# Performance work log

Measured on AMD Instinct MI355X. Metric: run time of the kernel, lower is better.

The kernel has to match this reference:

```python
import jax, jax.numpy as jnp
import numpy as np

N_NODES = 100000


def spmm(edge_src, edge_dst, edge_val, x):
    """z[dst] += val * x[src] over all edges (COO sparse-dense matmul)."""
    gathered = edge_val[:, None] * x[edge_src]  # [E, d]
    return jax.ops.segment_sum(gathered, edge_dst, num_segments=N_NODES)


def setup_inputs() -> dict:
    key = jax.random.key(0)
    k1, k2, k3, k4, k5, k6 = jax.random.split(key, 6)
    N, E, IN, H, C = N_NODES, 1600000, 256, 128, 40
    features = jax.random.normal(k1, (N, IN), dtype=jnp.float32)
    # xavier_uniform-like init
    b1 = float(np.sqrt(6.0 / (IN + H)))
    b2 = float(np.sqrt(6.0 / (H + C)))
    W1 = jax.random.uniform(k2, (IN, H), dtype=jnp.float32, minval=-b1, maxval=b1)
    W2 = jax.random.uniform(k3, (H, C), dtype=jnp.float32, minval=-b2, maxval=b2)
    edge_src = jax.random.randint(k4, (E,), 0, N, dtype=jnp.int32)
    edge_dst = jnp.sort(jax.random.randint(k5, (E,), 0, N, dtype=jnp.int32))
    # normalized-adjacency-like positive edge weights
    edge_val = jax.random.uniform(k6, (E,), dtype=jnp.float32)
    return {"features": features, "W1": W1, "W2": W2,
            "edge_src": edge_src, "edge_dst": edge_dst, "edge_val": edge_val}


def reference(features, W1, W2, edge_src, edge_dst, edge_val):
    # Decoupled GCN: all dense NN layers first (relu between, none after last) ...
    h = jax.nn.relu(features @ W1)
    h = h @ W2  # [N, num_classes]
    # ... then nlayers (=2) rounds of graph propagation (spmm aggregation)
    h = spmm(edge_src, edge_dst, edge_val, h)
    h = spmm(edge_src, edge_dst, edge_val, h)
    return h
```

## Files before the change

### kernel.cpp

```cpp
#include <hip/hip_runtime.h>
#include <cstddef>
#include <cstdint>

#define IN_DIM 256
#define H_DIM  128
#define C_DIM  40
#define BM     128
#define LDA    264
#define LDH    136
#define PAD_C  40
#define STEP   512

typedef short bf16x8 __attribute__((ext_vector_type(8)));
typedef float f32x16 __attribute__((ext_vector_type(16)));
typedef uint  u32x4  __attribute__((ext_vector_type(4)));

__device__ __forceinline__ ushort f2bf(float f) {
  uint u = __builtin_bit_cast(uint, f);
  u += 0x7fffu + ((u >> 16) & 1u);
  return (ushort)(u >> 16);
}
__device__ __forceinline__ float bf2f(uint s) {
  uint u = s << 16;
  return __builtin_bit_cast(float, u);
}
__device__ __forceinline__ uint pack2bf(float a, float b) {
#if __has_builtin(__builtin_amdgcn_cvt_pk_bf16_f32)
  typedef __bf16 bf16v2 __attribute__((ext_vector_type(2)));
  bf16v2 r = __builtin_amdgcn_cvt_pk_bf16_f32(a, b);
  return __builtin_bit_cast(uint, r);
#else
  return (uint)f2bf(a) | ((uint)f2bf(b) << 16);
#endif
}

__global__ void setup_kernel(const int* __restrict__ dst, int E,
                             int* __restrict__ row_ptr, int N,
                             const float* __restrict__ W1,
                             const float* __restrict__ W2,
                             ushort* __restrict__ b_frag,
                             ushort* __restrict__ w2f) {
  int tid = blockIdx.x * blockDim.x + threadIdx.x;
  if (tid < E) {
    int d1 = dst[tid];
    int d0 = (tid == 0) ? -1 : dst[tid - 1];
    for (int v = d0 + 1; v <= d1; ++v) row_ptr[v] = tid;
    if (tid == E - 1)
      for (int v = d1 + 1; v <= N; ++v) row_ptr[v] = E;
    return;
  }
  int u = tid - E;
  if (u < 4096) {
    int l = u & 63, ks = (u >> 6) & 15, tn = u >> 10;
    int n  = 32 * tn + (l & 31);
    int k0 = ks * 16 + ((l >> 5) << 3);
    ushort r[8];
#pragma unroll
    for (int j = 0; j < 8; ++j) r[j] = f2bf(W1[(k0 + j) * H_DIM + n]);
    *(uint4*)(b_frag + u * 8) = *(uint4*)r;
    return;
  }
  u -= 4096;
  if (u < 1024) {
    int l = u & 63, kt = u >> 6;
    int tn = kt & 1, kb = kt >> 1;
    int n  = 32 * tn + (l & 31);
    int k0 = kb * 16 + ((l >> 5) << 3);
    ushort r[8];
#pragma unroll
    for (int j = 0; j < 8; ++j)
      r[j] = (n < C_DIM) ? f2bf(W2[(k0 + j) * C_DIM + n]) : (ushort)0;
    *(uint4*)(w2f + u * 8) = *(uint4*)r;
  }
}

__global__ __launch_bounds__(256, 2) void fused_dense_kernel(
    const float* __restrict__ feat, const ushort* __restrict__ b_frag,
    const ushort* __restrict__ w2f, ushort* __restrict__ z0, int N) {
  __shared__ __align__(16) ushort smem[128 * LDA];

  const int t = threadIdx.x;
  const int w = t >> 6, l = t & 63;
  const int nb = blockIdx.x * BM;
  ushort* slab = smem + w * (32 * LDA);

  f32x16 acc[4];
#pragma unroll
  for (int tn = 0; tn < 4; ++tn)
#pragma unroll
    for (int r = 0; r < 16; ++r) acc[tn][r] = 0.f;

  const ushort* bp = b_frag + l * 8;
  bf16x8 Bx[2][4];
#pragma unroll
  for (int tn = 0; tn < 4; ++tn)
    Bx[0][tn] = *(const bf16x8*)(bp + tn * (16 * STEP));

#pragma unroll
  for (int c = 0; c < 32; ++c) {
    int grow = nb + 32 * w + c; if (grow >= N) grow = N - 1;
    float4 v = *(const float4*)(feat + (size_t)grow * IN_DIM + l * 4);
    uint2 pk;
    pk.x = pack2bf(v.x, v.y);
    pk.y = pack2bf(v.z, v.w);
    *(uint2*)(slab + c * LDA + l * 4) = pk;
  }

  const ushort* Abase = slab + (l & 31) * LDA + ((l >> 5) << 3);
#pragma unroll
  for (int ks = 0; ks < 16; ++ks) {
    const int c = ks & 1;
    if (ks < 15) {
#pragma unroll
      for (int tn = 0; tn < 4; ++tn)
        Bx[c ^ 1][tn] = *(const bf16x8*)(bp + tn * (16 * STEP) + (ks + 1) * STEP);
    }
    bf16x8 af = *(const bf16x8*)(Abase + ks * 16);
#pragma unroll
    for (int tn = 0; tn < 4; ++tn)
      acc[tn] = __builtin_amdgcn_mfma_f32_32x32x16_bf16(af, Bx[c][tn], acc[tn], 0, 0, 0);
  }

#pragma unroll
  for (int tn = 0; tn < 4; ++tn) {
    int col = tn * 32 + (l & 31);
#pragma unroll
    for (int r = 0; r < 16; ++r) {
      int nl = (r & 3) + 8 * (r >> 2) + 4 * (l >> 5);
      float v = acc[tn][r];
      slab[nl * LDH + col] = f2bf(v > 0.f ? v : 0.f);
    }
  }

  f32x16 acc2[2];
#pragma unroll
  for (int tn = 0; tn < 2; ++tn)
#pragma unroll
    for (int r = 0; r < 16; ++r) acc2[tn][r] = 0.f;

  const ushort* Hbase = slab + (l & 31) * LDH + ((l >> 5) << 3);
  const ushort* wp = w2f + l * 8;
#pragma unroll
  for (int kb = 0; kb < 8; ++kb) {
    bf16x8 af = *(const bf16x8*)(Hbase + kb * 16);
#pragma unroll
    for (int tn = 0; tn < 2; ++tn) {
      bf16x8 bfr = *(const bf16x8*)(wp + (kb * 2 + tn) * STEP);
      acc2[tn] = __builtin_amdgcn_mfma_f32_32x32x16_bf16(af, bfr, acc2[tn], 0, 0, 0);
    }
  }

#pragma unroll
  for (int tn = 0; tn < 2; ++tn) {
    int col = tn * 32 + (l & 31);
    if (col < C_DIM) {
#pragma unroll
      for (int r = 0; r < 16; ++r) {
        int node = nb + 32 * w + (r & 3) + 8 * (r >> 2) + 4 * (l >> 5);
        if (node < N) z0[(size_t)node * PAD_C + col] = f2bf(acc2[tn][r]);
      }
    }
  }
}

__global__ __launch_bounds__(256) void spmm_kernel(
    const int* __restrict__ row_ptr, const int* __restrict__ esrc,
    const float* __restrict__ eval, const ushort* __restrict__ x,
    ushort* __restrict__ zb, float* __restrict__ zf, int N, int out_f32) {
  int node = (blockIdx.x << 2) + (threadIdx.x >> 6);
  if (node >= N) return;
  const int lane = threadIdx.x & 63;
  const int h = lane >> 3;
  const int j = lane & 7;
  const bool act = (j < 5);

  int e   = row_ptr[node];
  int end = row_ptr[node + 1];

  float acc[8];
#pragma unroll
  for (int c = 0; c < 8; ++c) acc[c] = 0.f;

  for (; e + 16 <= end; e += 16) {
    int   s0 = esrc[e + h];
    int   s1 = esrc[e + 8 + h];
    float v0 = eval[e + h];
    float v1 = eval[e + 8 + h];
    if (act) {
      u32x4 a = *(const u32x4*)(x + (size_t)s0 * PAD_C + j * 8);
      u32x4 b = *(const u32x4*)(x + (size_t)s1 * PAD_C + j * 8);
      acc[0] = fmaf(v0, bf2f(a.x & 0xffffu), acc[0]);
      acc[1] = fmaf(v0, bf2f(a.x >> 16),     acc[1]);
      acc[2] = fmaf(v0, bf2f(a.y & 0xffffu), acc[2]);
      acc[3] = fmaf(v0, bf2f(a.y >> 16),     acc[3]);
      acc[4] = fmaf(v0, bf2f(a.z & 0xffffu), acc[4]);
      acc[5] = fmaf(v0, bf2f(a.z >> 16),     acc[5]);
      acc[6] = fmaf(v0, bf2f(a.w & 0xffffu), acc[6]);
      acc[7] = fmaf(v0, bf2f(a.w >> 16),     acc[7]);
      acc[0] = fmaf(v1, bf2f(b.x & 0xffffu), acc[0]);
      acc[1] = fmaf(v1, bf2f(b.x >> 16),     acc[1]);
      acc[2] = fmaf(v1, bf2f(b.y & 0xffffu), acc[2]);
      acc[3] = fmaf(v1, bf2f(b.y >> 16),     acc[3]);
      acc[4] = fmaf(v1, bf2f(b.z & 0xffffu), acc[4]);
      acc[5] = fmaf(v1, bf2f(b.z >> 16),     acc[5]);
      acc[6] = fmaf(v1, bf2f(b.w & 0xffffu), acc[6]);
      acc[7] = fmaf(v1, bf2f(b.w >> 16),     acc[7]);
    }
  }
  for (; e + 8 <= end; e += 8) {
    int   s = esrc[e + h];
    float v = eval[e + h];
    if (act) {
      u32x4 u = *(const u32x4*)(x + (size_t)s * PAD_C + j * 8);
      acc[0] = fmaf(v, bf2f(u.x & 0xffffu), acc[0]);
      acc[1] = fmaf(v, bf2f(u.x >> 16),     acc[1]);
      acc[2] = fmaf(v, bf2f(u.y & 0xffffu), acc[2]);
      acc[3] = fmaf(v, bf2f(u.y >> 16),     acc[3]);
      acc[4] = fmaf(v, bf2f(u.z & 0xffffu), acc[4]);
      acc[5] = fmaf(v, bf2f(u.z >> 16),     acc[5]);
      acc[6] = fmaf(v, bf2f(u.w & 0xffffu), acc[6]);
      acc[7] = fmaf(v, bf2f(u.w >> 16),     acc[7]);
    }
  }
  if (e < end) {
    int ei = e + h;
    int ec = ei < end ? ei : end - 1;
    int   s  = esrc[ec];
    float v0 = eval[ec];
    float v  = ei < end ? v0 : 0.f;
    if (act) {
      u32x4 u = *(const u32x4*)(x + (size_t)s * PAD_C + j * 8);
      acc[0] = fmaf(v, bf2f(u.x & 0xffffu), acc[0]);
      acc[1] = fmaf(v, bf2f(u.x >> 16),     acc[1]);
      acc[2] = fmaf(v, bf2f(u.y & 0xffffu), acc[2]);
      acc[3] = fmaf(v, bf2f(u.y >> 16),     acc[3]);
      acc[4] = fmaf(v, bf2f(u.z & 0xffffu), acc[4]);
      acc[5] = fmaf(v, bf2f(u.z >> 16),     acc[5]);
      acc[6] = fmaf(v, bf2f(u.w & 0xffffu), acc[6]);
      acc[7] = fmaf(v, bf2f(u.w >> 16),     acc[7]);
    }
  }

#pragma unroll
  for (int c = 0; c < 8; ++c) acc[c] += __shfl_xor(acc[c], 8);
#pragma unroll
  for (int c = 0; c < 8; ++c) acc[c] += __shfl_xor(acc[c], 16);
#pragma unroll
  for (int c = 0; c < 8; ++c) acc[c] += __shfl_xor(acc[c], 32);

  if (out_f32) {
    if (lane < 5) {
      float4 o0 = {acc[0], acc[1], acc[2], acc[3]};
      float4 o1 = {acc[4], acc[5], acc[6], acc[7]};
      float* p = zf + (size_t)node * C_DIM + j * 8;
      *(float4*)(p + 0) = o0;
      *(float4*)(p + 4) = o1;
    }
  } else {
    if (lane < 5) {
      uint4 p;
      p.x = (uint)f2bf(acc[0]) | ((uint)f2bf(acc[1]) << 16);
      p.y = (uint)f2bf(acc[2]) | ((uint)f2bf(acc[3]) << 16);
      p.z = (uint)f2bf(acc[4]) | ((uint)f2bf(acc[5]) << 16);
      p.w = (uint)f2bf(acc[6]) | ((uint)f2bf(acc[7]) << 16);
      *(uint4*)(zb + (size_t)node * PAD_C + j * 8) = p;
    }
  }
}

extern "C" void kernel_launch(void* const* d_in, const int* in_sizes, int n_in,
                              void* d_out, int out_size, void* d_ws, size_t ws_size,
                              hipStream_t stream) {
  const float* feat  = (const float*)d_in[0];
  const float* W1    = (const float*)d_in[1];
  const float* W2    = (const float*)d_in[2];
  const int*   esrc  = (const int*)d_in[3];
  const int*   edst  = (const int*)d_in[4];
  const float* evalp = (const float*)d_in[5];
  float* out = (float*)d_out;

  const int N = in_sizes[0] / IN_DIM;
  const int E = in_sizes[3];

  const int nblk = (N + BM - 1) / BM;

  char* ws = (char*)d_ws;
  ushort* z0     = (ushort*)ws;
  ushort* z1     = (ushort*)(ws + (size_t)N * PAD_C * 2);
  ushort* b_frag = (ushort*)(ws + (size_t)N * PAD_C * 4);
  ushort* w2f    = b_frag + 4 * 16 * STEP;
  int* row_ptr   = (int*)(w2f + 16 * STEP);

  const int setup_items = E + 4096 + 1024;
  setup_kernel<<<(setup_items + 255) / 256, 256, 0, stream>>>(
      edst, E, row_ptr, N, W1, W2, b_frag, w2f);
  fused_dense_kernel<<<nblk, 256, 0, stream>>>(feat, b_frag, w2f, z0, N);
  spmm_kernel<<<(N + 3) / 4, 256, 0, stream>>>(row_ptr, esrc, evalp, z0, z1, nullptr, N, 0);
  spmm_kernel<<<(N + 3) / 4, 256, 0, stream>>>(row_ptr, esrc, evalp, z1, nullptr, out, N, 1);
}
```

Baseline: 273.7 us.

## Split intermediate features into 64B-aligned and tail arrays; halve dense LDS footprint

The 40-column bf16 intermediate is stored as two arrays, a 32-column part (64-byte rows) and an 8-column part (16-byte rows), so each gathered row in the spmm kernels touches aligned cache-line segments instead of straddling 80-byte rows. The dense kernel now stages the feature tile in two K-halves with a smaller LDS slab, reusing it for the hidden activations, and raises the occupancy hint to 4 blocks per CU. Costs are a branch per gather lane and a second memory stream for the tail columns, plus more register pressure from the tighter launch bound.

```diff
diff --git a/kernel.cpp b/kernel.cpp
--- a/kernel.cpp
+++ b/kernel.cpp
@@ -6,9 +6,9 @@
 #define H_DIM  128
 #define C_DIM  40
 #define BM     128
-#define LDA    264
-#define LDH    136
-#define PAD_C  40
+#define LDAH   132
+#define XA_C   32
+#define XB_C   8
 #define STEP   512
 
 typedef short bf16x8 __attribute__((ext_vector_type(8)));
@@ -74,15 +74,16 @@
   }
 }
 
-__global__ __launch_bounds__(256, 2) void fused_dense_kernel(
+__global__ __launch_bounds__(256, 4) void fused_dense_kernel(
     const float* __restrict__ feat, const ushort* __restrict__ b_frag,
-    const ushort* __restrict__ w2f, ushort* __restrict__ z0, int N) {
-  __shared__ __align__(16) ushort smem[128 * LDA];
+    const ushort* __restrict__ w2f, ushort* __restrict__ z0a,
+    ushort* __restrict__ z0b, int N) {
+  __shared__ __align__(16) ushort smem[4 * 32 * LDAH];
 
   const int t = threadIdx.x;
   const int w = t >> 6, l = t & 63;
   const int nb = blockIdx.x * BM;
-  ushort* slab = smem + w * (32 * LDA);
+  ushort* slab = smem + w * (32 * LDAH);
 
   f32x16 acc[4];
 #pragma unroll
@@ -96,29 +97,34 @@
   for (int tn = 0; tn < 4; ++tn)
     Bx[0][tn] = *(const bf16x8*)(bp + tn * (16 * STEP));
 
-#pragma unroll
-  for (int c = 0; c < 32; ++c) {
-    int grow = nb + 32 * w + c; if (grow >= N) grow = N - 1;
-    float4 v = *(const float4*)(feat + (size_t)grow * IN_DIM + l * 4);
-    uint2 pk;
-    pk.x = pack2bf(v.x, v.y);
-    pk.y = pack2bf(v.z, v.w);
-    *(uint2*)(slab + c * LDA + l * 4) = pk;
-  }
-
-  const ushort* Abase = slab + (l & 31) * LDA + ((l >> 5) << 3);
-#pragma unroll
-  for (int ks = 0; ks < 16; ++ks) {
-    const int c = ks & 1;
-    if (ks < 15) {
+  const ushort* Abase = slab + (l & 31) * LDAH + ((l >> 5) << 3);
+
+#pragma unroll
+  for (int h = 0; h < 2; ++h) {
+#pragma unroll
+    for (int c = 0; c < 16; ++c) {
+      int r2 = 2 * c + (l >> 5);
+      int grow = nb + 32 * w + r2; if (grow >= N) grow = N - 1;
+      float4 v = *(const float4*)(feat + (size_t)grow * IN_DIM + h * 128 + (l & 31) * 4);
+      uint2 pk;
+      pk.x = pack2bf(v.x, v.y);
+      pk.y = pack2bf(v.z, v.w);
+      *(uint2*)(slab + r2 * LDAH + (l & 31) * 4) = pk;
+    }
+#pragma unroll
+    for (int kk = 0; kk < 8; ++kk) {
+      const int ks = h * 8 + kk;
+      const int c = ks & 1;
+      if (ks < 15) {
+#pragma unroll
+        for (int tn = 0; tn < 4; ++tn)
+          Bx[c ^ 1][tn] = *(const bf16x8*)(bp + tn * (16 * STEP) + (ks + 1) * STEP);
+      }
+      bf16x8 af = *(const bf16x8*)(Abase + kk * 16);
 #pragma unroll
       for (int tn = 0; tn < 4; ++tn)
-        Bx[c ^ 1][tn] = *(const bf16x8*)(bp + tn * (16 * STEP) + (ks + 1) * STEP);
-    }
-    bf16x8 af = *(const bf16x8*)(Abase + ks * 16);
-#pragma unroll
-    for (int tn = 0; tn < 4; ++tn)
-      acc[tn] = __builtin_amdgcn_mfma_f32_32x32x16_bf16(af, Bx[c][tn], acc[tn], 0, 0, 0);
+        acc[tn] = __builtin_amdgcn_mfma_f32_32x32x16_bf16(af, Bx[c][tn], acc[tn], 0, 0, 0);
+    }
   }
 
 #pragma unroll
@@ -128,7 +134,7 @@
     for (int r = 0; r < 16; ++r) {
       int nl = (r & 3) + 8 * (r >> 2) + 4 * (l >> 5);
       float v = acc[tn][r];
-      slab[nl * LDH + col] = f2bf(v > 0.f ? v : 0.f);
+      slab[nl * LDAH + col] = f2bf(v > 0.f ? v : 0.f);
     }
   }
 
@@ -138,7 +144,7 @@
 #pragma unroll
     for (int r = 0; r < 16; ++r) acc2[tn][r] = 0.f;
 
-  const ushort* Hbase = slab + (l & 31) * LDH + ((l >> 5) << 3);
+  const ushort* Hbase = slab + (l & 31) * LDAH + ((l >> 5) << 3);
   const ushort* wp = w2f + l * 8;
 #pragma unroll
   for (int kb = 0; kb < 8; ++kb) {
@@ -151,21 +157,20 @@
   }
 
 #pragma unroll
-  for (int tn = 0; tn < 2; ++tn) {
-    int col = tn * 32 + (l & 31);
-    if (col < C_DIM) {
-#pragma unroll
-      for (int r = 0; r < 16; ++r) {
-        int node = nb + 32 * w + (r & 3) + 8 * (r >> 2) + 4 * (l >> 5);
-        if (node < N) z0[(size_t)node * PAD_C + col] = f2bf(acc2[tn][r]);
-      }
+  for (int r = 0; r < 16; ++r) {
+    int node = nb + 32 * w + (r & 3) + 8 * (r >> 2) + 4 * (l >> 5);
+    if (node < N) {
+      z0a[(size_t)node * XA_C + (l & 31)] = f2bf(acc2[0][r]);
+      if ((l & 31) < XB_C)
+        z0b[(size_t)node * XB_C + (l & 31)] = f2bf(acc2[1][r]);
     }
   }
 }
 
 __global__ __launch_bounds__(256) void spmm_kernel(
     const int* __restrict__ row_ptr, const int* __restrict__ esrc,
-    const float* __restrict__ eval, const ushort* __restrict__ x,
+    const float* __restrict__ eval, const ushort* __restrict__ xa,
+    const ushort* __restrict__ xb, ushort* __restrict__ za,
     ushort* __restrict__ zb, float* __restrict__ zf, int N, int out_f32) {
   int node = (blockIdx.x << 2) + (threadIdx.x >> 6);
   if (node >= N) return;
@@ -187,8 +192,10 @@
     float v0 = eval[e + h];
     float v1 = eval[e + 8 + h];
     if (act) {
-      u32x4 a = *(const u32x4*)(x + (size_t)s0 * PAD_C + j * 8);
-      u32x4 b = *(const u32x4*)(x + (size_t)s1 * PAD_C + j * 8);
+      u32x4 a = (j < 4) ? *(const u32x4*)(xa + (size_t)s0 * XA_C + j * 8)
+                        : *(const u32x4*)(xb + (size_t)s0 * XB_C);
+      u32x4 b = (j < 4) ? *(const u32x4*)(xa + (size_t)s1 * XA_C + j * 8)
+                        : *(const u32x4*)(xb + (size_t)s1 * XB_C);
       acc[0] = fmaf(v0, bf2f(a.x & 0xffffu), acc[0]);
       acc[1] = fmaf(v0, bf2f(a.x >> 16),     acc[1]);
       acc[2] = fmaf(v0, bf2f(a.y & 0xffffu), acc[2]);
@@ -211,7 +218,8 @@
     int   s = esrc[e + h];
     float v = eval[e + h];
     if (act) {
-      u32x4 u = *(const u32x4*)(x + (size_t)s * PAD_C + j * 8);
+      u32x4 u = (j < 4) ? *(const u32x4*)(xa + (size_t)s * XA_C + j * 8)
+                        : *(const u32x4*)(xb + (size_t)s * XB_C);
       acc[0] = fmaf(v, bf2f(u.x & 0xffffu), acc[0]);
       acc[1] = fmaf(v, bf2f(u.x >> 16),     acc[1]);
       acc[2] = fmaf(v, bf2f(u.y & 0xffffu), acc[2]);
@@ -229,7 +237,8 @@
     float v0 = eval[ec];
     float v  = ei < end ? v0 : 0.f;
     if (act) {
-      u32x4 u = *(const u32x4*)(x + (size_t)s * PAD_C + j * 8);
+      u32x4 u = (j < 4) ? *(const u32x4*)(xa + (size_t)s * XA_C + j * 8)
+                        : *(const u32x4*)(xb + (size_t)s * XB_C);
       acc[0] = fmaf(v, bf2f(u.x & 0xffffu), acc[0]);
       acc[1] = fmaf(v, bf2f(u.x >> 16),     acc[1]);
       acc[2] = fmaf(v, bf2f(u.y & 0xffffu), acc[2]);
@@ -263,7 +272,8 @@
       p.y = (uint)f2bf(acc[2]) | ((uint)f2bf(acc[3]) << 16);
       p.z = (uint)f2bf(acc[4]) | ((uint)f2bf(acc[5]) << 16);
       p.w = (uint)f2bf(acc[6]) | ((uint)f2bf(acc[7]) << 16);
-      *(uint4*)(zb + (size_t)node * PAD_C + j * 8) = p;
+      if (j < 4) *(uint4*)(za + (size_t)node * XA_C + j * 8) = p;
+      else       *(uint4*)(zb + (size_t)node * XB_C) = p;
     }
   }
 }
@@ -285,16 +295,20 @@
   const int nblk = (N + BM - 1) / BM;
 
   char* ws = (char*)d_ws;
-  ushort* z0     = (ushort*)ws;
-  ushort* z1     = (ushort*)(ws + (size_t)N * PAD_C * 2);
-  ushort* b_frag = (ushort*)(ws + (size_t)N * PAD_C * 4);
+  ushort* z0a    = (ushort*)ws;
+  ushort* z0b    = z0a + (size_t)N * XA_C;
+  ushort* z1a    = z0b + (size_t)N * XB_C;
+  ushort* z1b    = z1a + (size_t)N * XA_C;
+  ushort* b_frag = z1b + (size_t)N * XB_C;
   ushort* w2f    = b_frag + 4 * 16 * STEP;
   int* row_ptr   = (int*)(w2f + 16 * STEP);
 
   const int setup_items = E + 4096 + 1024;
   setup_kernel<<<(setup_items + 255) / 256, 256, 0, stream>>>(
       edst, E, row_ptr, N, W1, W2, b_frag, w2f);
-  fused_dense_kernel<<<nblk, 256, 0, stream>>>(feat, b_frag, w2f, z0, N);
-  spmm_kernel<<<(N + 3) / 4, 256, 0, stream>>>(row_ptr, esrc, evalp, z0, z1, nullptr, N, 0);
-  spmm_kernel<<<(N + 3) / 4, 256, 0, stream>>>(row_ptr, esrc, evalp, z1, nullptr, out, N, 1);
-}
+  fused_dense_kernel<<<nblk, 256, 0, stream>>>(feat, b_frag, w2f, z0a, z0b, N);
+  spmm_kernel<<<(N + 3) / 4, 256, 0, stream>>>(row_ptr, esrc, evalp, z0a, z0b,
+                                               z1a, z1b, nullptr, N, 0);
+  spmm_kernel<<<(N + 3) / 4, 256, 0, stream>>>(row_ptr, esrc, evalp, z1a, z1b,
+                                               nullptr, nullptr, out, N, 1);
+}
```

Measured after the change: 281.6 us. 1.03x slower.

## Stream feature K-chunks through a smaller LDS slab and raise occupancy

Applied to the files above, without the earlier changes.

The dense kernel now stages the 256-wide feature row in four 64-column chunks through a 68-stride LDS slab instead of holding the whole 264-stride tile. The next chunk's global loads are issued while the MFMAs for the current chunk run. The hidden activations are also written and consumed in two 64-column halves. Shrinking LDS lets the launch bound request 4 blocks per CU instead of 2. The risks are more register pressure from the prefetch buffers and extra LDS writes, and there is no barrier, so correctness depends on each wave reading and writing only its own slab.

```diff
diff --git a/kernel.cpp b/kernel.cpp
--- a/kernel.cpp
+++ b/kernel.cpp
@@ -6,8 +6,7 @@
 #define H_DIM  128
 #define C_DIM  40
 #define BM     128
-#define LDA    264
-#define LDH    136
+#define LDQ    68
 #define PAD_C  40
 #define STEP   512
 
@@ -74,15 +73,18 @@
   }
 }
 
-__global__ __launch_bounds__(256, 2) void fused_dense_kernel(
+__global__ __launch_bounds__(256, 4) void fused_dense_kernel(
     const float* __restrict__ feat, const ushort* __restrict__ b_frag,
     const ushort* __restrict__ w2f, ushort* __restrict__ z0, int N) {
-  __shared__ __align__(16) ushort smem[128 * LDA];
+  __shared__ __align__(16) ushort smem[4 * 32 * LDQ];
 
   const int t = threadIdx.x;
   const int w = t >> 6, l = t & 63;
   const int nb = blockIdx.x * BM;
-  ushort* slab = smem + w * (32 * LDA);
+  ushort* slab = smem + w * (32 * LDQ);
+
+  const int sr = l >> 4;
+  const int sc = l & 15;
 
   f32x16 acc[4];
 #pragma unroll
@@ -96,39 +98,60 @@
   for (int tn = 0; tn < 4; ++tn)
     Bx[0][tn] = *(const bf16x8*)(bp + tn * (16 * STEP));
 
-#pragma unroll
-  for (int c = 0; c < 32; ++c) {
-    int grow = nb + 32 * w + c; if (grow >= N) grow = N - 1;
-    float4 v = *(const float4*)(feat + (size_t)grow * IN_DIM + l * 4);
+  const float* fbase = feat + (size_t)(nb + 32 * w) * IN_DIM + sc * 4;
+
+  float4 pre[8];
+#pragma unroll
+  for (int c = 0; c < 8; ++c) {
+    int grow = nb + 32 * w + 4 * c + sr;
+    const float* p = fbase + (size_t)(4 * c + sr) * IN_DIM;
+    if (grow >= N) p = feat + (size_t)(N - 1) * IN_DIM + sc * 4;
+    pre[c] = *(const float4*)(p);
+  }
+#pragma unroll
+  for (int c = 0; c < 8; ++c) {
     uint2 pk;
-    pk.x = pack2bf(v.x, v.y);
-    pk.y = pack2bf(v.z, v.w);
-    *(uint2*)(slab + c * LDA + l * 4) = pk;
-  }
-
-  const ushort* Abase = slab + (l & 31) * LDA + ((l >> 5) << 3);
-#pragma unroll
-  for (int ks = 0; ks < 16; ++ks) {
-    const int c = ks & 1;
-    if (ks < 15) {
+    pk.x = pack2bf(pre[c].x, pre[c].y);
+    pk.y = pack2bf(pre[c].z, pre[c].w);
+    *(uint2*)(slab + (4 * c + sr) * LDQ + sc * 4) = pk;
+  }
+
+  const ushort* Abase = slab + (l & 31) * LDQ + ((l >> 5) << 3);
+
+#pragma unroll
+  for (int q = 0; q < 4; ++q) {
+#pragma unroll
+    for (int ks = 0; ks < 4; ++ks) {
+      const int gks = 4 * q + ks;
+      const int c = gks & 1;
+      if (gks < 15) {
+#pragma unroll
+        for (int tn = 0; tn < 4; ++tn)
+          Bx[c ^ 1][tn] = *(const bf16x8*)(bp + tn * (16 * STEP) + (gks + 1) * STEP);
+      }
+      if (q < 3) {
+#pragma unroll
+        for (int d = 0; d < 2; ++d) {
+          const int cc = 2 * ks + d;
+          int grow = nb + 32 * w + 4 * cc + sr;
+          const float* p = fbase + (size_t)(4 * cc + sr) * IN_DIM + (q + 1) * 64;
+          if (grow >= N) p = feat + (size_t)(N - 1) * IN_DIM + sc * 4 + (q + 1) * 64;
+          pre[cc] = *(const float4*)(p);
+        }
+      }
+      bf16x8 af = *(const bf16x8*)(Abase + ks * 16);
 #pragma unroll
       for (int tn = 0; tn < 4; ++tn)
-        Bx[c ^ 1][tn] = *(const bf16x8*)(bp + tn * (16 * STEP) + (ks + 1) * STEP);
-    }
-    bf16x8 af = *(const bf16x8*)(Abase + ks * 16);
-#pragma unroll
-    for (int tn = 0; tn < 4; ++tn)
-      acc[tn] = __builtin_amdgcn_mfma_f32_32x32x16_bf16(af, Bx[c][tn], acc[tn], 0, 0, 0);
-  }
-
-#pragma unroll
-  for (int tn = 0; tn < 4; ++tn) {
-    int col = tn * 32 + (l & 31);
-#pragma unroll
-    for (int r = 0; r < 16; ++r) {
-      int nl = (r & 3) + 8 * (r >> 2) + 4 * (l >> 5);
-      float v = acc[tn][r];
-      slab[nl * LDH + col] = f2bf(v > 0.f ? v : 0.f);
+        acc[tn] = __builtin_amdgcn_mfma_f32_32x32x16_bf16(af, Bx[c][tn], acc[tn], 0, 0, 0);
+    }
+    if (q < 3) {
+#pragma unroll
+      for (int c = 0; c < 8; ++c) {
+        uint2 pk;
+        pk.x = pack2bf(pre[c].x, pre[c].y);
+        pk.y = pack2bf(pre[c].z, pre[c].w);
+        *(uint2*)(slab + (4 * c + sr) * LDQ + sc * 4) = pk;
+      }
     }
   }
 
@@ -138,15 +161,29 @@
 #pragma unroll
     for (int r = 0; r < 16; ++r) acc2[tn][r] = 0.f;
 
-  const ushort* Hbase = slab + (l & 31) * LDH + ((l >> 5) << 3);
+  const ushort* Hbase = slab + (l & 31) * LDQ + ((l >> 5) << 3);
   const ushort* wp = w2f + l * 8;
-#pragma unroll
-  for (int kb = 0; kb < 8; ++kb) {
-    bf16x8 af = *(const bf16x8*)(Hbase + kb * 16);
-#pragma unroll
-    for (int tn = 0; tn < 2; ++tn) {
-      bf16x8 bfr = *(const bf16x8*)(wp + (kb * 2 + tn) * STEP);
-      acc2[tn] = __builtin_amdgcn_mfma_f32_32x32x16_bf16(af, bfr, acc2[tn], 0, 0, 0);
+
+#pragma unroll
+  for (int hc = 0; hc < 2; ++hc) {
+#pragma unroll
+    for (int tn = 2 * hc; tn < 2 * hc + 2; ++tn) {
+      int col = (tn - 2 * hc) * 32 + (l & 31);
+#pragma unroll
+      for (int r = 0; r < 16; ++r) {
+        int nl = (r & 3) + 8 * (r >> 2) + 4 * (l >> 5);
+        float v = acc[tn][r];
+        slab[nl * LDQ + col] = f2bf(v > 0.f ? v : 0.f);
+      }
+    }
+#pragma unroll
+    for (int kb = 4 * hc; kb < 4 * hc + 4; ++kb) {
+      bf16x8 af = *(const bf16x8*)(Hbase + (kb - 4 * hc) * 16);
+#pragma unroll
+      for (int tn = 0; tn < 2; ++tn) {
+        bf16x8 bfr = *(const bf16x8*)(wp + (kb * 2 + tn) * STEP);
+        acc2[tn] = __builtin_amdgcn_mfma_f32_32x32x16_bf16(af, bfr, acc2[tn], 0, 0, 0);
+      }
     }
   }
 
```

Measured after the change: 272.9 us. No clear change (-0.3%).
